# Performance work log

Hardware: AMD Instinct MI355X
Metric: run time of the kernel (lower is better)

Reference implementation:

```python
import jax, jax.numpy as jnp
import numpy as np

DIM = 512
NUM_HEADS = 4
SCALE = 1.0 / np.sqrt(DIM)  # note: module scales by 1/sqrt(dim), not 1/sqrt(head_dim)


def setup_inputs() -> dict:
    key = jax.random.key(0)
    k1, k2, k3, k4, k5, k6 = jax.random.split(key, 6)
    B, N, M, C = 8, 2048, 2048, DIM
    bound = 1.0 / np.sqrt(C)
    return {
        "F1": jax.random.normal(k1, (B, N, C), dtype=jnp.float32),
        "F2": jax.random.normal(k2, (B, M, C), dtype=jnp.float32),
        "W_qkv": jax.random.uniform(k3, (C, C), jnp.float32, -bound, bound),
        "b_qkv": jax.random.uniform(k4, (C,), jnp.float32, -bound, bound),
        "W_proj": jax.random.uniform(k5, (C, C), jnp.float32, -bound, bound),
        "b_proj": jax.random.uniform(k6, (C,), jnp.float32, -bound, bound),
    }


def reference(F1, F2, W_qkv, b_qkv, W_proj, b_proj):
    B, N, C = F1.shape
    M = F2.shape[1]
    H, D = NUM_HEADS, C // NUM_HEADS
    # shared qkv projection (same weights for q, k and v in the original module)
    q = (F1 @ W_qkv + b_qkv).reshape(B, N, H, D)  # queries from F1
    kv = (F2 @ W_qkv + b_qkv).reshape(B, M, H, D)  # keys == values from F2
    attn = jnp.einsum("bnhd,bmhd->bhnm", q * SCALE, kv)
    attn = jax.nn.softmax(attn, axis=-1)
    x = jnp.einsum("bhnm,bmhd->bnhd", attn, kv).reshape(B, N, C)
    return x @ W_proj + b_proj
```

## Files before the change

kernel.cpp:

```cpp
#include <hip/hip_runtime.h>
#include <math.h>


typedef __attribute__((ext_vector_type(8))) short s16x8;
typedef __attribute__((ext_vector_type(4))) float f32x4;

#define C_DIM 512
#define HDIM  128
#define NROWS 16384
#define SCALE_Q 0.04419417382415922f
#define LOG2E   1.4426950408889634f

__device__ __forceinline__ unsigned short f2bf(float f) {
    union { float f; unsigned u; } v; v.f = f;
    unsigned r = v.u + 0x7fffu + ((v.u >> 16) & 1u);
    return (unsigned short)(r >> 16);
}

__device__ __forceinline__ void async16(const void* g, void* l) {
    __builtin_amdgcn_global_load_lds(
        (const __attribute__((address_space(1))) void*)g,
        (__attribute__((address_space(3))) void*)l, 16, 0, 0);
}

__global__ __launch_bounds__(256)
void conv_bf16_2(const float* __restrict__ s0, const float* __restrict__ s1,
                 unsigned short* __restrict__ d0, unsigned short* __restrict__ d1,
                 int n8) {
    const float* src = blockIdx.y ? s1 : s0;
    unsigned short* dst = blockIdx.y ? d1 : d0;
    int i = blockIdx.x * 256 + threadIdx.x;
    if (i >= n8) return;
    float4 a = ((const float4*)src)[2 * i];
    float4 b = ((const float4*)src)[2 * i + 1];
    union { unsigned short us[8]; uint4 v; } o;
    o.us[0] = f2bf(a.x); o.us[1] = f2bf(a.y); o.us[2] = f2bf(a.z); o.us[3] = f2bf(a.w);
    o.us[4] = f2bf(b.x); o.us[5] = f2bf(b.y); o.us[6] = f2bf(b.z); o.us[7] = f2bf(b.w);
    ((uint4*)dst)[i] = o.v;
}

__global__ __launch_bounds__(256)
void wconv_t2(const float* __restrict__ W0, const float* __restrict__ W1,
              unsigned short* __restrict__ T0, unsigned short* __restrict__ T1) {
    const float* W = blockIdx.z ? W1 : W0;
    unsigned short* Wt = blockIdx.z ? T1 : T0;
    __shared__ float t[64][65];
    const int k0 = blockIdx.y * 64, n0 = blockIdx.x * 64;
    const int c = threadIdx.x & 63, r0 = threadIdx.x >> 6;
#pragma unroll
    for (int r = r0; r < 64; r += 4)
        t[r][c] = W[(size_t)(k0 + r) * C_DIM + n0 + c];
    __syncthreads();
#pragma unroll
    for (int r = r0; r < 64; r += 4)
        Wt[(size_t)(n0 + r) * C_DIM + k0 + c] = f2bf(t[c][r]);
}

template <int OUT_BF16>
__global__ __launch_bounds__(256, 3)
void gemm_bt(const unsigned short* __restrict__ A,
             const unsigned short* __restrict__ Bt,
             const float* __restrict__ bias,
             void* __restrict__ Cv, float oscTop, int topRows) {
    __shared__ __align__(16) unsigned short As[128][64];
    __shared__ __align__(16) unsigned short Bs[128][64];

    const int tid  = threadIdx.x;
    const int wid  = tid >> 6;
    const int lane = tid & 63;
    const int lr   = lane & 15;
    const int quad = lane >> 4;
    const int wm   = wid >> 1;
    const int wn   = wid & 1;
    const int rowBase = blockIdx.y * 128;
    const int colBase = blockIdx.x * 128;
    const int srow = lane >> 3;
    const int soff = srow * C_DIM + (((lane & 7) ^ (srow & 7)) * 8);
    const float osc = (rowBase < topRows) ? oscTop : 1.0f;

    f32x4 acc[4][4];
#pragma unroll
    for (int i = 0; i < 4; i++)
#pragma unroll
        for (int j = 0; j < 4; j++) acc[i][j] = (f32x4)0.0f;

    for (int kt = 0; kt < 8; kt++) {
        const int k0 = kt * 64;
        __syncthreads();
#pragma unroll
        for (int i = 0; i < 4; i++) {
            const int R = wid * 32 + i * 8;
            async16(A  + (size_t)(rowBase + R) * C_DIM + k0 + soff, &As[R][0]);
            async16(Bt + (size_t)(colBase + R) * C_DIM + k0 + soff, &Bs[R][0]);
        }
        __syncthreads();

#pragma unroll
        for (int s = 0; s < 2; s++) {
            s16x8 af[4], bf[4];
#pragma unroll
            for (int i = 0; i < 4; i++)
                af[i] = *(const s16x8*)&As[wm * 64 + i * 16 + lr][((s * 4 + quad) ^ (lr & 7)) * 8];
#pragma unroll
            for (int j = 0; j < 4; j++)
                bf[j] = *(const s16x8*)&Bs[wn * 64 + j * 16 + lr][((s * 4 + quad) ^ (lr & 7)) * 8];
#pragma unroll
            for (int i = 0; i < 4; i++)
#pragma unroll
                for (int j = 0; j < 4; j++)
                    acc[i][j] = __builtin_amdgcn_mfma_f32_16x16x32_bf16(af[i], bf[j], acc[i][j], 0, 0, 0);
        }
    }

    float bcol[4];
#pragma unroll
    for (int j = 0; j < 4; j++)
        bcol[j] = bias[colBase + wn * 64 + j * 16 + lr];
#pragma unroll
    for (int i = 0; i < 4; i++) {
#pragma unroll
        for (int j = 0; j < 4; j++) {
            const int col = colBase + wn * 64 + j * 16 + lr;
#pragma unroll
            for (int r = 0; r < 4; r++) {
                const int row = rowBase + wm * 64 + i * 16 + quad * 4 + r;
                float v = (acc[i][j][r] + bcol[j]) * osc;
                if (OUT_BF16)
                    ((unsigned short*)Cv)[(size_t)row * C_DIM + col] = f2bf(v);
                else
                    ((float*)Cv)[(size_t)row * C_DIM + col] = v;
            }
        }
    }
}

__global__ __launch_bounds__(256, 3)
void cross_attn(const unsigned short* __restrict__ Q,
                const unsigned short* __restrict__ KV,
                unsigned short* __restrict__ X) {
    __shared__ __align__(16) unsigned short Kt[64][128];
    __shared__ __align__(16) unsigned short Vt[128][72];
    __shared__ __align__(16) unsigned short Pl[4][32][72];

    const int tid  = threadIdx.x;
    const int wid  = tid >> 6;
    const int lane = tid & 63;
    const int lr   = lane & 15;
    const int quad = lane >> 4;
    const int b    = blockIdx.z;
    const int h    = blockIdx.y;
    const int hoff = h * HDIM;
    const int kap  = lr * 4 + quad;
    const int l7   = lane & 7;
    const size_t qrow0  = (size_t)b * 2048 + blockIdx.x * 128 + wid * 32;
    const size_t kvrow0 = (size_t)b * 2048;

    s16x8 qf[2][4];
#pragma unroll
    for (int i = 0; i < 2; i++)
#pragma unroll
        for (int kk = 0; kk < 4; kk++)
            qf[i][kk] = *(const s16x8*)(Q + (qrow0 + i * 16 + lr) * C_DIM + hoff + kk * 32 + quad * 8);

    f32x4 O[2][8];
#pragma unroll
    for (int i = 0; i < 2; i++)
#pragma unroll
        for (int dt = 0; dt < 8; dt++) O[i][dt] = (f32x4)0.0f;
    float lacc[2][4];
#pragma unroll
    for (int i = 0; i < 2; i++)
#pragma unroll
        for (int r = 0; r < 4; r++) lacc[i][r] = 0.0f;

    for (int kt = 0; kt < 32; kt++) {
        const int key0 = kt * 64;
        __syncthreads();
#pragma unroll
        for (int i = 0; i < 4; i++) {
            const int dc = wid + 4 * i;
            uint4 v = *(const uint4*)(KV + (kvrow0 + key0 + kap) * C_DIM + hoff + dc * 8);
            *(uint4*)&Kt[lane][(dc ^ l7) * 8] = v;
            const unsigned short* e = (const unsigned short*)&v;
#pragma unroll
            for (int t = 0; t < 8; t++) Vt[dc * 8 + t][kap] = e[t];
        }
        __syncthreads();

        f32x4 s[2][4];
#pragma unroll
        for (int i = 0; i < 2; i++)
#pragma unroll
            for (int j = 0; j < 4; j++) s[i][j] = (f32x4)0.0f;
#pragma unroll
        for (int kk = 0; kk < 4; kk++) {
#pragma unroll
            for (int j = 0; j < 4; j++) {
                s16x8 kf = *(const s16x8*)&Kt[j * 16 + lr][((kk * 4 + quad) ^ (lr & 7)) * 8];
                s[0][j] = __builtin_amdgcn_mfma_f32_16x16x32_bf16(qf[0][kk], kf, s[0][j], 0, 0, 0);
                s[1][j] = __builtin_amdgcn_mfma_f32_16x16x32_bf16(qf[1][kk], kf, s[1][j], 0, 0, 0);
            }
        }

#pragma unroll
        for (int i = 0; i < 2; i++) {
#pragma unroll
            for (int r = 0; r < 4; r++) {
                float p0 = exp2f(s[i][0][r]);
                float p1 = exp2f(s[i][1][r]);
                float p2 = exp2f(s[i][2][r]);
                float p3 = exp2f(s[i][3][r]);
                lacc[i][r] += (p0 + p1) + (p2 + p3);
                uint2 pk;
                pk.x = (unsigned)f2bf(p0) | ((unsigned)f2bf(p1) << 16);
                pk.y = (unsigned)f2bf(p2) | ((unsigned)f2bf(p3) << 16);
                *(uint2*)&Pl[wid][i * 16 + quad * 4 + r][4 * lr] = pk;
            }
        }

#pragma unroll
        for (int kk = 0; kk < 2; kk++) {
            s16x8 pa0 = *(const s16x8*)&Pl[wid][lr][kk * 32 + quad * 8];
            s16x8 pa1 = *(const s16x8*)&Pl[wid][16 + lr][kk * 32 + quad * 8];
#pragma unroll
            for (int dt = 0; dt < 8; dt++) {
                s16x8 vf = *(const s16x8*)&Vt[dt * 16 + lr][kk * 32 + quad * 8];
                O[0][dt] = __builtin_amdgcn_mfma_f32_16x16x32_bf16(pa0, vf, O[0][dt], 0, 0, 0);
                O[1][dt] = __builtin_amdgcn_mfma_f32_16x16x32_bf16(pa1, vf, O[1][dt], 0, 0, 0);
            }
        }
    }

#pragma unroll
    for (int i = 0; i < 2; i++) {
#pragma unroll
        for (int r = 0; r < 4; r++) {
            float l = lacc[i][r];
#pragma unroll
            for (int off = 1; off < 16; off <<= 1)
                l += __shfl_xor(l, off);
            const float inv = 1.0f / l;
            const size_t row = (qrow0 + i * 16 + quad * 4 + r) * C_DIM + hoff;
#pragma unroll
            for (int dt = 0; dt < 8; dt++)
                X[row + dt * 16 + lr] = f2bf(O[i][dt][r] * inv);
        }
    }
}

extern "C" void kernel_launch(void* const* d_in, const int* in_sizes, int n_in,
                              void* d_out, int out_size, void* d_ws, size_t ws_size,
                              hipStream_t stream) {
    const float* F1     = (const float*)d_in[0];
    const float* F2     = (const float*)d_in[1];
    const float* W_qkv  = (const float*)d_in[2];
    const float* b_qkv  = (const float*)d_in[3];
    const float* W_proj = (const float*)d_in[4];
    const float* b_proj = (const float*)d_in[5];
    float* out = (float*)d_out;

    const size_t NC = (size_t)NROWS * C_DIM;
    unsigned short* F1b = (unsigned short*)d_ws;
    unsigned short* F2b = F1b + NC;
    unsigned short* Qw  = F2b + NC;
    unsigned short* KVw = Qw  + NC;
    unsigned short* Wqt = KVw + NC;
    unsigned short* Wpt = Wqt + C_DIM * C_DIM;
    unsigned short* Xw  = F1b;

    dim3 blk(256);

    conv_bf16_2<<<dim3(NC / 8 / 256, 2), blk, 0, stream>>>(F1, F2, F1b, F2b, (int)(NC / 8));
    wconv_t2<<<dim3(8, 8, 2), blk, 0, stream>>>(W_qkv, W_proj, Wqt, Wpt);

    gemm_bt<1><<<dim3(4, 256), blk, 0, stream>>>(F1b, Wqt, b_qkv, Qw, SCALE_Q * LOG2E, NROWS);
    cross_attn<<<dim3(16, 4, 8), blk, 0, stream>>>(Qw, KVw, Xw);
    gemm_bt<0><<<dim3(4, 128), blk, 0, stream>>>(Xw, Wpt, b_proj, out, 1.0f, 0);
}
```

Measured before the change: 283.9 us.

## Pre-transpose KV into a separate buffer and load K/V tiles via async global-to-LDS

Adds a kv_transpose kernel that writes a per-(batch,head) transposed copy of KV, so the attention kernel no longer scatters V element by element into LDS. K and V tiles are now fetched with global_load_lds async copies, using XOR-swizzled addresses to avoid bank conflicts, and the V read pattern is updated to match. This removes the costly per-element LDS transposition and register round-trip in the inner loop. In exchange it adds an extra kernel launch and an extra read and write of the full KV tensor, and reuses the F2b buffer as scratch.

```diff
diff --git a/kernel.cpp b/kernel.cpp
--- a/kernel.cpp
+++ b/kernel.cpp
@@ -56,6 +56,26 @@
         Wt[(size_t)(n0 + r) * C_DIM + k0 + c] = f2bf(t[c][r]);
 }
 
+__global__ __launch_bounds__(256)
+void kv_transpose(const unsigned short* __restrict__ KV,
+                  unsigned short* __restrict__ KVT) {
+    __shared__ unsigned short t[64][66];
+    const int key0 = blockIdx.x * 64;
+    const int d0   = blockIdx.y * 64;
+    const int bh   = blockIdx.z;
+    const int b    = bh >> 2, h = bh & 3;
+    const int c = threadIdx.x & 63, r0 = threadIdx.x >> 6;
+    const unsigned short* src = KV + ((size_t)(b * 2048 + key0)) * C_DIM + h * HDIM + d0;
+#pragma unroll
+    for (int r = r0; r < 64; r += 4)
+        t[r][c] = src[(size_t)r * C_DIM + c];
+    __syncthreads();
+    unsigned short* dst = KVT + ((size_t)(bh * HDIM + d0)) * 2048 + key0;
+#pragma unroll
+    for (int r = r0; r < 64; r += 4)
+        dst[(size_t)r * 2048 + c] = t[c][r];
+}
+
 template <int OUT_BF16>
 __global__ __launch_bounds__(256, 3)
 void gemm_bt(const unsigned short* __restrict__ A,
@@ -137,9 +157,10 @@
 __global__ __launch_bounds__(256, 3)
 void cross_attn(const unsigned short* __restrict__ Q,
                 const unsigned short* __restrict__ KV,
+                const unsigned short* __restrict__ KVT,
                 unsigned short* __restrict__ X) {
     __shared__ __align__(16) unsigned short Kt[64][128];
-    __shared__ __align__(16) unsigned short Vt[128][72];
+    __shared__ __align__(16) unsigned short Vt[128][64];
     __shared__ __align__(16) unsigned short Pl[4][32][72];
 
     const int tid  = threadIdx.x;
@@ -150,8 +171,6 @@
     const int b    = blockIdx.z;
     const int h    = blockIdx.y;
     const int hoff = h * HDIM;
-    const int kap  = lr * 4 + quad;
-    const int l7   = lane & 7;
     const size_t qrow0  = (size_t)b * 2048 + blockIdx.x * 128 + wid * 32;
     const size_t kvrow0 = (size_t)b * 2048;
 
@@ -162,6 +181,20 @@
         for (int kk = 0; kk < 4; kk++)
             qf[i][kk] = *(const s16x8*)(Q + (qrow0 + i * 16 + lr) * C_DIM + hoff + kk * 32 + quad * 8);
 
+    const unsigned short* pK[4];
+    const unsigned short* pV[4];
+#pragma unroll
+    for (int a = 0; a < 4; a++) {
+        const int rk  = a * 4 + (lane >> 4);
+        const int p   = lane & 15;
+        const int ck  = (p & 8) | ((p ^ (rk & 7)) & 7);
+        const int key = 4 * rk + wid;
+        pK[a] = KV + (kvrow0 + key) * C_DIM + hoff + ck * 8;
+        const int d  = wid * 32 + a * 8 + (lane >> 3);
+        const int cv = (lane & 7) ^ (lane >> 3);
+        pV[a] = KVT + ((size_t)((b * 4 + h) * HDIM + d)) * 2048 + cv * 8;
+    }
+
     f32x4 O[2][8];
 #pragma unroll
     for (int i = 0; i < 2; i++)
@@ -174,16 +207,12 @@
         for (int r = 0; r < 4; r++) lacc[i][r] = 0.0f;
 
     for (int kt = 0; kt < 32; kt++) {
-        const int key0 = kt * 64;
+        const size_t key0 = (size_t)kt * 64;
         __syncthreads();
 #pragma unroll
-        for (int i = 0; i < 4; i++) {
-            const int dc = wid + 4 * i;
-            uint4 v = *(const uint4*)(KV + (kvrow0 + key0 + kap) * C_DIM + hoff + dc * 8);
-            *(uint4*)&Kt[lane][(dc ^ l7) * 8] = v;
-            const unsigned short* e = (const unsigned short*)&v;
-#pragma unroll
-            for (int t = 0; t < 8; t++) Vt[dc * 8 + t][kap] = e[t];
+        for (int a = 0; a < 4; a++) {
+            async16(pK[a] + key0 * C_DIM, &Kt[wid * 16 + a * 4][0]);
+            async16(pV[a] + key0,         &Vt[wid * 32 + a * 8][0]);
         }
         __syncthreads();
 
@@ -224,7 +253,7 @@
             s16x8 pa1 = *(const s16x8*)&Pl[wid][16 + lr][kk * 32 + quad * 8];
 #pragma unroll
             for (int dt = 0; dt < 8; dt++) {
-                s16x8 vf = *(const s16x8*)&Vt[dt * 16 + lr][kk * 32 + quad * 8];
+                s16x8 vf = *(const s16x8*)&Vt[dt * 16 + lr][((kk * 4 + quad) ^ (lr & 7)) * 8];
                 O[0][dt] = __builtin_amdgcn_mfma_f32_16x16x32_bf16(pa0, vf, O[0][dt], 0, 0, 0);
                 O[1][dt] = __builtin_amdgcn_mfma_f32_16x16x32_bf16(pa1, vf, O[1][dt], 0, 0, 0);
             }
@@ -267,6 +296,7 @@
     unsigned short* Wqt = KVw + NC;
     unsigned short* Wpt = Wqt + C_DIM * C_DIM;
     unsigned short* Xw  = F1b;
+    unsigned short* KVT = F2b;
 
     dim3 blk(256);
 
@@ -274,6 +304,7 @@
     wconv_t2<<<dim3(8, 8, 2), blk, 0, stream>>>(W_qkv, W_proj, Wqt, Wpt);
 
     gemm_bt<1><<<dim3(4, 256), blk, 0, stream>>>(F1b, Wqt, b_qkv, Qw, SCALE_Q * LOG2E, NROWS);
-    cross_attn<<<dim3(16, 4, 8), blk, 0, stream>>>(Qw, KVw, Xw);
+    kv_transpose<<<dim3(32, 2, 32), blk, 0, stream>>>(KVw, KVT);
+    cross_attn<<<dim3(16, 4, 8), blk, 0, stream>>>(Qw, KVw, KVT, Xw);
     gemm_bt<0><<<dim3(4, 128), blk, 0, stream>>>(Xw, Wpt, b_proj, out, 1.0f, 0);
 }
```

Result: slower. 309.1 us (+8.9%).
